# Optimization experiments

Measured on AMD Instinct MI355X. Metric: run time of the kernel, lower is better.

## Reference

```python
import jax, jax.numpy as jnp
import numpy as np

RADIUS_VIEWPOOL = 0.075  # self.view_pool_radius
EPS_BN = 1e-5


def _pconv(x, w, b):
    # 1x1 Conv1d: x (B, Cin, N), w (Cout, Cin), b (Cout,)
    return jnp.einsum('oc,bcn->bon', w, x) + b[None, :, None]


def _bn(x, p):
    # eval-mode BatchNorm1d; p rows: gamma, beta, running_mean, running_var
    g, b, m, v = p[0], p[1], p[2], p[3]
    inv = g * jax.lax.rsqrt(v + EPS_BN)
    return (x - m[None, :, None]) * inv[None, :, None] + b[None, :, None]


def setup_inputs() -> dict:
    key = jax.random.key(0)
    it = iter(jax.random.split(key, 80))
    Np, Nr = 16384, 8192
    inp = {}
    inp['pcd_xyz'] = jax.random.uniform(next(it), (1, Np, 3), jnp.float32)
    inp['rgb_xyz'] = jax.random.uniform(next(it), (1, Nr, 3), jnp.float32)
    inp['pcd_features'] = jax.random.normal(next(it), (1, 32, Np), jnp.float32)
    inp['rgb_features'] = jax.random.normal(next(it), (1, 128, Nr), jnp.float32)

    def conv(name, o, c):
        s = 1.0 / np.sqrt(c)
        inp[name + '_w'] = jax.random.uniform(next(it), (o, c), jnp.float32, -s, s)
        inp[name + '_b'] = jax.random.uniform(next(it), (o,), jnp.float32, -s, s)

    def bn(name, c):
        g = 1.0 + 0.1 * jax.random.normal(next(it), (c,), jnp.float32)
        b = 0.1 * jax.random.normal(next(it), (c,), jnp.float32)
        m = 0.1 * jax.random.normal(next(it), (c,), jnp.float32)
        v = jax.random.uniform(next(it), (c,), jnp.float32, 0.5, 1.5)
        inp[name] = jnp.stack([g, b, m, v])

    conv('cc1', 384, 384); bn('cc_bn', 384); conv('cc2', 128, 384)
    conv('co1', 256, 256); bn('co_bn', 256); conv('co2', 128, 256)
    conv('dh1', 160, 160); bn('dh1_bn', 160)
    conv('dh2', 160, 160); bn('dh2_bn', 160)
    conv('dh3', 128, 160)
    conv('sh1', 128, 128); bn('sh_bn', 128)
    conv('sh2', 1, 128)
    return inp


def _forward(pcd_xyz, rgb_xyz, pcd_features, rgb_features,
             cc1_w, cc1_b, cc_bn, cc2_w, cc2_b,
             co1_w, co1_b, co_bn, co2_w, co2_b,
             dh1_w, dh1_b, dh1_bn, dh2_w, dh2_b, dh2_bn, dh3_w, dh3_b,
             sh1_w, sh1_b, sh_bn, sh2_w, sh2_b):
    Np = pcd_xyz.shape[1]
    Nr = rgb_xyz.shape[1]
    C_rgb = rgb_features.shape[1]

    # ---- three_nn: 3 nearest rgb points for each pcd point ----
    d2 = jnp.sum((pcd_xyz[0, :, None, :] - rgb_xyz[0, None, :, :]) ** 2, axis=-1)  # (Np, Nr)
    neg_d2, idx = jax.lax.top_k(-d2, 3)                     # (Np, 3)
    dist = jnp.sqrt(jnp.maximum(-neg_d2, 0.0))
    # idx[dist > radius] = -1 in torch -> indexes shadow (zero) row appended at end
    neighbor = jnp.where(dist > RADIUS_VIEWPOOL, Nr, idx)   # (Np, 3)

    rgb_f = jnp.concatenate([rgb_features[0].T,
                             jnp.zeros((1, C_rgb), rgb_features.dtype)], axis=0)  # (Nr+1, 128)
    nf = rgb_f[neighbor]                                    # (Np, 3, 128) gather
    max_features = nf.max(axis=1)                           # (Np, 128)

    # fuception fusion: conv over concatenated neighbor features, then fuse with max
    x_cat = nf.reshape(Np, 3 * C_rgb).T[None]               # (1, 384, Np)
    h = jax.nn.relu(_bn(_pconv(x_cat, cc1_w, cc1_b), cc_bn))
    concat_out = _pconv(h, cc2_w, cc2_b)                    # (1, 128, Np)
    x2 = jnp.concatenate([concat_out, max_features.T[None]], axis=1)  # (1, 256, Np)
    h = jax.nn.relu(_bn(_pconv(x2, co1_w, co1_b), co_bn))
    attach = _pconv(h, co2_w, co2_b)                        # (1, 128, Np)

    # fuse pcd + assigned rgb features -> direct feature header (160 = 128+32)
    full = jnp.concatenate([pcd_features, attach], axis=1)  # (1, 160, Np)
    h = jax.nn.relu(_bn(_pconv(full, dh1_w, dh1_b), dh1_bn))
    h = jax.nn.relu(_bn(_pconv(h, dh2_w, dh2_b), dh2_bn))
    fp = _pconv(h, dh3_w, dh3_b)                            # (1, 128, Np)

    # score header: conv-bn-relu-conv-sigmoid
    s = jax.nn.relu(_bn(_pconv(fp, sh1_w, sh1_b), sh_bn))
    vote_scores = jax.nn.sigmoid(_pconv(s, sh2_w, sh2_b))[0, 0]  # (Np,)

    # L2-normalized vote features (N, 128)
    vf = fp[0].T
    vf = vf / jnp.maximum(jnp.linalg.norm(vf, axis=1, keepdims=True), 1e-12)
    return pcd_xyz[0], vote_scores, vf


def reference(pcd_xyz, rgb_xyz, pcd_features, rgb_features,
              cc1_w, cc1_b, cc_bn, cc2_w, cc2_b,
              co1_w, co1_b, co_bn, co2_w, co2_b,
              dh1_w, dh1_b, dh1_bn, dh2_w, dh2_b, dh2_bn, dh3_w, dh3_b,
              sh1_w, sh1_b, sh_bn, sh2_w, sh2_b):
    return _forward(pcd_xyz, rgb_xyz, pcd_features, rgb_features,
                    cc1_w, cc1_b, cc_bn, cc2_w, cc2_b,
                    co1_w, co1_b, co_bn, co2_w, co2_b,
                    dh1_w, dh1_b, dh1_bn, dh2_w, dh2_b, dh2_bn, dh3_w, dh3_b,
                    sh1_w, sh1_b, sh_bn, sh2_w, sh2_b)
```

## Files before the change

kernel.cpp:

```cpp
#include <hip/hip_runtime.h>
#include <math.h>

#define NP 16384
#define NR 8192
#define GRID 13
#define NCELL (GRID * GRID * GRID)
#define CAP 28

typedef __attribute__((ext_vector_type(8))) short short8;
typedef __attribute__((ext_vector_type(4))) float f32x4;

__device__ inline unsigned short f2b(float f) {
  unsigned int x = __float_as_uint(f);
  return (unsigned short)((x + 0x7FFFu + ((x >> 16) & 1u)) >> 16);
}
__device__ inline float blo(unsigned int u) { return __uint_as_float(u << 16); }
__device__ inline float bhi(unsigned int u) { return __uint_as_float(u & 0xffff0000u); }

__global__ __launch_bounds__(256) void k_pre(const float* __restrict__ rf,
                                             const float* __restrict__ rxyz,
                                             const float* __restrict__ pf,
                                             const float* __restrict__ s0, const float* __restrict__ s1,
                                             const float* __restrict__ s2, const float* __restrict__ s3,
                                             const float* __restrict__ s4, const float* __restrict__ s5,
                                             const float* __restrict__ s6, const float* __restrict__ s7,
                                             unsigned short* __restrict__ rgbTb,
                                             float4* __restrict__ rxyz4,
                                             unsigned short* __restrict__ fullp,
                                             unsigned short* __restrict__ dst,
                                             int* __restrict__ cellCnt) {
  __shared__ float tile[128][65];
  int b = blockIdx.x, t = threadIdx.x;
  if (b < 128) {
    int r0 = b * 64;
    for (int e = 0; e < 32; ++e) {
      int idx = t + e * 256;
      int c = idx >> 6, rl = idx & 63;
      tile[c][rl] = rf[c * NR + r0 + rl];
    }
    __syncthreads();
    for (int e = 0; e < 32; ++e) {
      int idx = t + e * 256;
      int rl = idx >> 7, c = idx & 127;
      rgbTb[(size_t)(r0 + rl) * 128 + c] = f2b(tile[c][rl]);
    }
    if (b == 0 && t < 128) rgbTb[(size_t)NR * 128 + t] = 0;
    if ((t >> 6) == 0) {
      int i = r0 + (t & 63);
      float x = rxyz[i * 3], y = rxyz[i * 3 + 1], z = rxyz[i * 3 + 2];
      rxyz4[i] = make_float4(x, y, z, fmaf(x, x, fmaf(y, y, z * z)));
    }
  } else if (b < 384) {
    int n0 = (b - 128) * 64;
    for (int e = 0; e < 8; ++e) {
      int idx = t + e * 256;
      int c = idx >> 6, nl = idx & 63;
      tile[c][nl] = pf[c * NP + n0 + nl];
    }
    __syncthreads();
    for (int e = 0; e < 8; ++e) {
      int idx = t + e * 256;
      int nl = idx >> 5, c = idx & 31;
      fullp[(size_t)(n0 + nl) * 32 + c] = f2b(tile[c][nl]);
    }
  } else if (b < 960) {
    const int groups[8] = {18432, 6144, 8192, 4096, 3200, 3200, 2560, 2048};
    const int Cs[8]     = {384, 384, 256, 256, 160, 160, 160, 128};
    const int offs[8]   = {0, 147456, 196608, 262144, 294912, 320512, 346112, 366592};
    const float* srcs[8] = {s0, s1, s2, s3, s4, s5, s6, s7};
    int j = b - 384;
    int m = j / 72, bx = j % 72;
    int gidx = bx * 256 + t;
    if (gidx >= groups[m]) return;
    int C = Cs[m], NC = C >> 5;
    int ot = gidx / (NC * 64);
    int rem = gidx - ot * (NC * 64);
    int k = rem >> 6, lane = rem & 63;
    int q = lane >> 4, l15 = lane & 15;
    const float* sp = srcs[m] + (size_t)(ot * 16 + l15) * C + k * 32 + q * 8;
    float4 a = *(const float4*)sp, c4 = *(const float4*)(sp + 4);
    uint4 o;
    o.x = f2b(a.x) | ((unsigned int)f2b(a.y) << 16);
    o.y = f2b(a.z) | ((unsigned int)f2b(a.w) << 16);
    o.z = f2b(c4.x) | ((unsigned int)f2b(c4.y) << 16);
    o.w = f2b(c4.z) | ((unsigned int)f2b(c4.w) << 16);
    *(uint4*)(dst + offs[m] + (size_t)gidx * 8) = o;
  } else {
    int idx = (b - 960) * 256 + t;
    if (idx < NCELL) cellCnt[idx] = 0;
  }
}

__global__ __launch_bounds__(64) void k_build(const float4* __restrict__ rxyz4,
                                              int* __restrict__ cellCnt,
                                              float4* __restrict__ cellTab) {
  int i = blockIdx.x * 64 + threadIdx.x;
  float4 r = rxyz4[i];
  int cx = (int)(r.x * 13.f); cx = cx < 0 ? 0 : (cx > 12 ? 12 : cx);
  int cy = (int)(r.y * 13.f); cy = cy < 0 ? 0 : (cy > 12 ? 12 : cy);
  int cz = (int)(r.z * 13.f); cz = cz < 0 ? 0 : (cz > 12 ? 12 : cz);
  int cell = (cz * 13 + cy) * 13 + cx;
  int slot = atomicAdd(&cellCnt[cell], 1);
  if (slot < CAP) cellTab[(size_t)cell * CAP + slot] = make_float4(r.x, r.y, r.z, __int_as_float(i));
}

__global__ __launch_bounds__(64) void k_nn_grid(const float* __restrict__ pxyz,
                                                const int* __restrict__ cellCnt,
                                                const float4* __restrict__ cellTab,
                                                int* __restrict__ nbr) {
  int n = blockIdx.x * 64 + threadIdx.x;
  float px = pxyz[n * 3], py = pxyz[n * 3 + 1], pz = pxyz[n * 3 + 2];
  int cx = (int)(px * 13.f); cx = cx < 0 ? 0 : (cx > 12 ? 12 : cx);
  int cy = (int)(py * 13.f); cy = cy < 0 ? 0 : (cy > 12 ? 12 : cy);
  int cz = (int)(pz * 13.f); cz = cz < 0 ? 0 : (cz > 12 ? 12 : cz);
  const float R2L = 0.005626125f;
  unsigned long long k0, k1, k2;
  k0 = k1 = k2 = ((unsigned long long)__float_as_uint(R2L) << 32);
  int x0 = cx > 0 ? cx - 1 : 0, x1 = cx < 12 ? cx + 1 : 12;
  int y0 = cy > 0 ? cy - 1 : 0, y1 = cy < 12 ? cy + 1 : 12;
  int z0 = cz > 0 ? cz - 1 : 0, z1 = cz < 12 ? cz + 1 : 12;
  for (int zz = z0; zz <= z1; ++zz)
    for (int yy = y0; yy <= y1; ++yy) {
      int cb = (zz * 13 + yy) * 13;
      for (int xx = x0; xx <= x1; ++xx) {
        int c = cb + xx;
        int m = cellCnt[c]; m = m < CAP ? m : CAP;
        const float4* tp = cellTab + (size_t)c * CAP;
        for (int k = 0; k < m; ++k) {
          float4 q = tp[k];
          float dx = q.x - px, dy = q.y - py, dz = q.z - pz;
          float d2 = fmaf(dx, dx, fmaf(dy, dy, dz * dz));
          unsigned long long key =
              ((unsigned long long)__float_as_uint(d2) << 32) | (unsigned int)__float_as_int(q.w);
          if (key < k2) {
            if (key < k1) {
              k2 = k1;
              if (key < k0) { k1 = k0; k0 = key; }
              else          { k1 = key; }
            } else k2 = key;
          }
        }
      }
    }
  const float R2 = 0.075f * 0.075f;
  float d0 = __uint_as_float((unsigned int)(k0 >> 32));
  float d1 = __uint_as_float((unsigned int)(k1 >> 32));
  float d2v = __uint_as_float((unsigned int)(k2 >> 32));
  int j0 = (d0 > R2) ? NR : (int)(k0 & 0xffffffffu);
  int j1 = (d1 > R2) ? NR : (int)(k1 & 0xffffffffu);
  int j2 = (d2v > R2) ? NR : (int)(k2 & 0xffffffffu);
  nbr[n * 3 + 0] = j0; nbr[n * 3 + 1] = j1; nbr[n * 3 + 2] = j2;
}

template <int C, int O, int COFF, bool BN, bool RELU>
__device__ __forceinline__ void mlp_layer(const unsigned short* __restrict__ W,
                                          const float* __restrict__ bias,
                                          const float* __restrict__ bnp,
                                          const unsigned short* Xs,
                                          unsigned short* Ys,
                                          int wo, int q, int l15, int lane) {
  constexpr int NC = C / 32;
  constexpr int NT = O / 16;
  constexpr int MT = (NT + 7) / 8;
  f32x4 acc[MT][2];
  short8 afb[2][MT];
  const unsigned short* wp[MT];
#pragma unroll
  for (int i = 0; i < MT; ++i) {
    acc[i][0] = (f32x4){0.f, 0.f, 0.f, 0.f};
    acc[i][1] = (f32x4){0.f, 0.f, 0.f, 0.f};
    int ot = wo + i * 8;
    wp[i] = W + ((size_t)(((ot < NT) ? ot : 0) * NC) * 64 + lane) * 8;
  }
#pragma unroll
  for (int k = 0; k < 2 && k < NC; ++k)
#pragma unroll
    for (int i = 0; i < MT; ++i)
      if (wo + i * 8 < NT) afb[k][i] = *(const short8*)(wp[i] + (size_t)k * 512);
  short8 bf0 = *(const short8*)&Xs[l15 * 392 + q * 8];
  short8 bf1 = *(const short8*)&Xs[(16 + l15) * 392 + q * 8];
#pragma unroll
  for (int k = 0; k < NC; ++k) {
    short8 nbf0 = bf0, nbf1 = bf1;
    if (k + 1 < NC) {
      nbf0 = *(const short8*)&Xs[l15 * 392 + (k + 1) * 32 + q * 8];
      nbf1 = *(const short8*)&Xs[(16 + l15) * 392 + (k + 1) * 32 + q * 8];
    }
    int slot = k & 1;
#pragma unroll
    for (int i = 0; i < MT; ++i) {
      if (wo + i * 8 < NT) {
        acc[i][0] = __builtin_amdgcn_mfma_f32_16x16x32_bf16(afb[slot][i], bf0, acc[i][0], 0, 0, 0);
        acc[i][1] = __builtin_amdgcn_mfma_f32_16x16x32_bf16(afb[slot][i], bf1, acc[i][1], 0, 0, 0);
      }
    }
    if (k + 2 < NC) {
#pragma unroll
      for (int i = 0; i < MT; ++i)
        if (wo + i * 8 < NT) afb[slot][i] = *(const short8*)(wp[i] + (size_t)(k + 2) * 512);
    }
    bf0 = nbf0; bf1 = nbf1;
  }
#pragma unroll
  for (int i = 0; i < MT; ++i) {
    int ot = wo + i * 8;
    if (ot >= NT) continue;
    int o4 = ot * 16 + q * 4;
    f32x4 bb = *(const f32x4*)(bias + o4);
    f32x4 sc, sh;
    if (BN) {
      f32x4 g  = *(const f32x4*)(bnp + o4);
      f32x4 be = *(const f32x4*)(bnp + O + o4);
      f32x4 mm = *(const f32x4*)(bnp + 2 * O + o4);
      f32x4 vv = *(const f32x4*)(bnp + 3 * O + o4);
#pragma unroll
      for (int r = 0; r < 4; ++r) {
        float inv = g[r] * rsqrtf(vv[r] + 1e-5f);
        sc[r] = inv; sh[r] = (bb[r] - mm[r]) * inv + be[r];
      }
    } else {
      sc = (f32x4){1.f, 1.f, 1.f, 1.f}; sh = bb;
    }
#pragma unroll
    for (int rt = 0; rt < 2; ++rt) {
      ushort4 u;
#pragma unroll
      for (int r = 0; r < 4; ++r) {
        float x = acc[i][rt][r] * sc[r] + sh[r];
        if (RELU) x = fmaxf(x, 0.f);
        ((unsigned short*)&u)[r] = f2b(x);
      }
      *(ushort4*)&Ys[(rt * 16 + l15) * 392 + COFF + ot * 16 + q * 4] = u;
    }
  }
}

__global__ __launch_bounds__(512) void k_mlp(
    const unsigned short* __restrict__ rgbTb,
    const int* __restrict__ nbr,
    const unsigned short* __restrict__ fullp,
    const unsigned short* __restrict__ wcc1, const unsigned short* __restrict__ wcc2,
    const unsigned short* __restrict__ wco1, const unsigned short* __restrict__ wco2,
    const unsigned short* __restrict__ wdh1, const unsigned short* __restrict__ wdh2,
    const unsigned short* __restrict__ wdh3, const unsigned short* __restrict__ wsh1,
    const float* __restrict__ cc1_b, const float* __restrict__ cc_bn,
    const float* __restrict__ cc2_b,
    const float* __restrict__ co1_b, const float* __restrict__ co_bn,
    const float* __restrict__ co2_b,
    const float* __restrict__ dh1_b, const float* __restrict__ dh1_bn,
    const float* __restrict__ dh2_b, const float* __restrict__ dh2_bn,
    const float* __restrict__ dh3_b,
    const float* __restrict__ sh1_b, const float* __restrict__ sh_bn,
    const float* __restrict__ sh2_w, const float* __restrict__ sh2_b,
    const float* __restrict__ pxyz, float* __restrict__ out) {
  __shared__ unsigned short Ab[32 * 392];
  __shared__ unsigned short Bb[32 * 392];
  int t = threadIdx.x, lane = t & 63, w = t >> 6;
  int wo = w & 7;
  int q = lane >> 4, l15 = lane & 15;
  int n0 = blockIdx.x * 32;
  unsigned int mreg[4];
#pragma unroll
  for (int pj = 0; pj < 4; ++pj) {
    int r = w * 4 + pj;
    int n = n0 + r;
    int j0 = nbr[n * 3 + 0], j1 = nbr[n * 3 + 1], j2 = nbr[n * 3 + 2];
    unsigned int a = ((const unsigned int*)(rgbTb + (size_t)j0 * 128))[lane];
    unsigned int b = ((const unsigned int*)(rgbTb + (size_t)j1 * 128))[lane];
    unsigned int c = ((const unsigned int*)(rgbTb + (size_t)j2 * 128))[lane];
    unsigned int* xr = (unsigned int*)&Ab[r * 392];
    xr[lane] = a; xr[64 + lane] = b; xr[128 + lane] = c;
    float ml = fmaxf(blo(a), fmaxf(blo(b), blo(c)));
    float mh = fmaxf(bhi(a), fmaxf(bhi(b), bhi(c)));
    mreg[pj] = (__float_as_uint(mh) & 0xffff0000u) | (__float_as_uint(ml) >> 16);
  }
  __syncthreads();
  mlp_layer<384, 384, 0, true,  true >(wcc1, cc1_b, cc_bn, Ab, Bb, wo, q, l15, lane);
  __syncthreads();
#pragma unroll
  for (int pj = 0; pj < 4; ++pj)
    ((unsigned int*)&Ab[(w * 4 + pj) * 392])[64 + lane] = mreg[pj];
  mlp_layer<384, 128, 0, false, false>(wcc2, cc2_b, nullptr, Bb, Ab, wo, q, l15, lane);
  __syncthreads();
  mlp_layer<256, 256, 0, true,  true >(wco1, co1_b, co_bn, Ab, Bb, wo, q, l15, lane);
  __syncthreads();
  mlp_layer<256, 128, 32, false, false>(wco2, co2_b, nullptr, Bb, Ab, wo, q, l15, lane);
  for (int idx = t; idx < 128; idx += 512) {
    int row = idx >> 2, c8 = idx & 3;
    *(uint4*)&Ab[row * 392 + c8 * 8] = *(const uint4*)(fullp + (size_t)(n0 + row) * 32 + c8 * 8);
  }
  __syncthreads();
  mlp_layer<160, 160, 0, true,  true >(wdh1, dh1_b, dh1_bn, Ab, Bb, wo, q, l15, lane);
  __syncthreads();
  mlp_layer<160, 160, 0, true,  true >(wdh2, dh2_b, dh2_bn, Bb, Ab, wo, q, l15, lane);
  __syncthreads();
  mlp_layer<160, 128, 0, false, false>(wdh3, dh3_b, nullptr, Ab, Bb, wo, q, l15, lane);
  __syncthreads();
  mlp_layer<128, 128, 0, true,  true >(wsh1, sh1_b, sh_bn, Bb, Ab, wo, q, l15, lane);
  __syncthreads();
  int col8 = (lane & 15) * 8;
  float4 w0 = *(const float4*)(sh2_w + col8);
  float4 wA = *(const float4*)(sh2_w + col8 + 4);
  float bvv = sh2_b[0];
  int row = w * 4 + (lane >> 4);
  uint4 raw = *(const uint4*)&Ab[row * 392 + col8];
  float acc = blo(raw.x) * w0.x + bhi(raw.x) * w0.y + blo(raw.y) * w0.z + bhi(raw.y) * w0.w +
              blo(raw.z) * wA.x + bhi(raw.z) * wA.y + blo(raw.w) * wA.z + bhi(raw.w) * wA.w;
  acc += __shfl_xor(acc, 1); acc += __shfl_xor(acc, 2);
  acc += __shfl_xor(acc, 4); acc += __shfl_xor(acc, 8);
  if ((lane & 15) == 0) out[49152 + n0 + row] = 1.f / (1.f + expf(-(acc + bvv)));
  uint4 rf = *(const uint4*)&Bb[row * 392 + col8];
  float v[8] = {blo(rf.x), bhi(rf.x), blo(rf.y), bhi(rf.y),
                blo(rf.z), bhi(rf.z), blo(rf.w), bhi(rf.w)};
  float s = 0.f;
#pragma unroll
  for (int i = 0; i < 8; ++i) s = fmaf(v[i], v[i], s);
  s += __shfl_xor(s, 1); s += __shfl_xor(s, 2);
  s += __shfl_xor(s, 4); s += __shfl_xor(s, 8);
  float inv = 1.f / fmaxf(sqrtf(s), 1e-12f);
  float* op = out + 65536 + (size_t)(n0 + row) * 128 + col8;
  *(float4*)op = make_float4(v[0] * inv, v[1] * inv, v[2] * inv, v[3] * inv);
  *(float4*)(op + 4) = make_float4(v[4] * inv, v[5] * inv, v[6] * inv, v[7] * inv);
  for (int i = t; i < 96; i += 512) out[n0 * 3 + i] = pxyz[n0 * 3 + i];
}

extern "C" void kernel_launch(void* const* d_in, const int* in_sizes, int n_in,
                              void* d_out, int out_size, void* d_ws, size_t ws_size,
                              hipStream_t stream) {
  const float* pcd_xyz = (const float*)d_in[0];
  const float* rgb_xyz = (const float*)d_in[1];
  const float* pcd_f   = (const float*)d_in[2];
  const float* rgb_f   = (const float*)d_in[3];
  const float* cc1_w = (const float*)d_in[4];  const float* cc1_b = (const float*)d_in[5];
  const float* cc_bn = (const float*)d_in[6];
  const float* cc2_w = (const float*)d_in[7];  const float* cc2_b = (const float*)d_in[8];
  const float* co1_w = (const float*)d_in[9];  const float* co1_b = (const float*)d_in[10];
  const float* co_bn = (const float*)d_in[11];
  const float* co2_w = (const float*)d_in[12]; const float* co2_b = (const float*)d_in[13];
  const float* dh1_w = (const float*)d_in[14]; const float* dh1_b = (const float*)d_in[15];
  const float* dh1_bn = (const float*)d_in[16];
  const float* dh2_w = (const float*)d_in[17]; const float* dh2_b = (const float*)d_in[18];
  const float* dh2_bn = (const float*)d_in[19];
  const float* dh3_w = (const float*)d_in[20]; const float* dh3_b = (const float*)d_in[21];
  const float* sh1_w = (const float*)d_in[22]; const float* sh1_b = (const float*)d_in[23];
  const float* sh_bn = (const float*)d_in[24];
  const float* sh2_w = (const float*)d_in[25]; const float* sh2_b = (const float*)d_in[26];

  char* ws = (char*)d_ws;
  float* out = (float*)d_out;

  unsigned short* wb    = (unsigned short*)(ws);
  unsigned short* rgbTb = (unsigned short*)(ws + 0x100000);
  float4* rxyz4         = (float4*)(ws + 0x320000);
  int*    nbr           = (int*)(ws + 0x400000);
  int*    cellCnt       = (int*)(ws + 0x480000);
  float4* cellTab       = (float4*)(ws + 0x490000);
  unsigned short* fullp = (unsigned short*)(ws + 0xA00000);

  unsigned short* wb_cc1 = wb;
  unsigned short* wb_cc2 = wb + 147456;
  unsigned short* wb_co1 = wb + 196608;
  unsigned short* wb_co2 = wb + 262144;
  unsigned short* wb_dh1 = wb + 294912;
  unsigned short* wb_dh2 = wb + 320512;
  unsigned short* wb_dh3 = wb + 346112;
  unsigned short* wb_sh1 = wb + 366592;

  k_pre<<<969, 256, 0, stream>>>(rgb_f, rgb_xyz, pcd_f,
                                 cc1_w, cc2_w, co1_w, co2_w, dh1_w, dh2_w, dh3_w, sh1_w,
                                 rgbTb, rxyz4, fullp, wb, cellCnt);
  k_build<<<128, 64, 0, stream>>>(rxyz4, cellCnt, cellTab);
  k_nn_grid<<<256, 64, 0, stream>>>(pcd_xyz, cellCnt, cellTab, nbr);
  k_mlp<<<512, 512, 0, stream>>>(rgbTb, nbr, fullp,
                                 wb_cc1, wb_cc2, wb_co1, wb_co2,
                                 wb_dh1, wb_dh2, wb_dh3, wb_sh1,
                                 cc1_b, cc_bn, cc2_b, co1_b, co_bn, co2_b,
                                 dh1_b, dh1_bn, dh2_b, dh2_bn, dh3_b,
                                 sh1_b, sh_bn, sh2_w, sh2_b,
                                 pcd_xyz, out);
}
```

Before: 188.7 us.

## Split grid neighbor search across 8 lanes per point with shuffle top-3 merge

The three-nearest-neighbor grid search now gives each query point 8 threads, each scanning a strided subset of the up to 27 neighboring cells, then merges the per-lane top-3 keys with xor shuffles. The goal is more parallelism and latency hiding in a kernel that previously launched only 16384 threads with long serial loops. In exchange it adds shuffle-merge overhead, imbalanced work per lane, and redundant coordinate loads. It also drops the unused squared-norm component and clamps neighbor indices before the feature gather.

```diff
diff --git a/kernel.cpp b/kernel.cpp
--- a/kernel.cpp
+++ b/kernel.cpp
@@ -48,7 +48,7 @@
     if ((t >> 6) == 0) {
       int i = r0 + (t & 63);
       float x = rxyz[i * 3], y = rxyz[i * 3 + 1], z = rxyz[i * 3 + 2];
-      rxyz4[i] = make_float4(x, y, z, fmaf(x, x, fmaf(y, y, z * z)));
+      rxyz4[i] = make_float4(x, y, z, 0.f);
     }
   } else if (b < 384) {
     int n0 = (b - 128) * 64;
@@ -104,34 +104,37 @@
   if (slot < CAP) cellTab[(size_t)cell * CAP + slot] = make_float4(r.x, r.y, r.z, __int_as_float(i));
 }
 
-__global__ __launch_bounds__(64) void k_nn_grid(const float* __restrict__ pxyz,
-                                                const int* __restrict__ cellCnt,
-                                                const float4* __restrict__ cellTab,
-                                                int* __restrict__ nbr) {
-  int n = blockIdx.x * 64 + threadIdx.x;
+__global__ __launch_bounds__(256) void k_nn_grid(const float* __restrict__ pxyz,
+                                                 const int* __restrict__ cellCnt,
+                                                 const float4* __restrict__ cellTab,
+                                                 int* __restrict__ nbr) {
+  int tid = blockIdx.x * 256 + threadIdx.x;
+  int n = tid >> 3, sub = tid & 7;
   float px = pxyz[n * 3], py = pxyz[n * 3 + 1], pz = pxyz[n * 3 + 2];
   int cx = (int)(px * 13.f); cx = cx < 0 ? 0 : (cx > 12 ? 12 : cx);
   int cy = (int)(py * 13.f); cy = cy < 0 ? 0 : (cy > 12 ? 12 : cy);
   int cz = (int)(pz * 13.f); cz = cz < 0 ? 0 : (cz > 12 ? 12 : cz);
   const float R2L = 0.005626125f;
-  unsigned long long k0, k1, k2;
-  k0 = k1 = k2 = ((unsigned long long)__float_as_uint(R2L) << 32);
-  int x0 = cx > 0 ? cx - 1 : 0, x1 = cx < 12 ? cx + 1 : 12;
-  int y0 = cy > 0 ? cy - 1 : 0, y1 = cy < 12 ? cy + 1 : 12;
-  int z0 = cz > 0 ? cz - 1 : 0, z1 = cz < 12 ? cz + 1 : 12;
-  for (int zz = z0; zz <= z1; ++zz)
-    for (int yy = y0; yy <= y1; ++yy) {
+  const unsigned long long SENT = ((unsigned long long)__float_as_uint(R2L) << 32);
+  unsigned long long k0 = SENT, k1 = SENT, k2 = SENT;
+  int vi = 0;
+  for (int dz = -1; dz <= 1; ++dz) {
+    int zz = cz + dz; if ((unsigned)zz > 12u) continue;
+    for (int dy = -1; dy <= 1; ++dy) {
+      int yy = cy + dy; if ((unsigned)yy > 12u) continue;
       int cb = (zz * 13 + yy) * 13;
-      for (int xx = x0; xx <= x1; ++xx) {
+      for (int dx = -1; dx <= 1; ++dx) {
+        int xx = cx + dx; if ((unsigned)xx > 12u) continue;
+        if (((vi++) & 7) != sub) continue;
         int c = cb + xx;
         int m = cellCnt[c]; m = m < CAP ? m : CAP;
         const float4* tp = cellTab + (size_t)c * CAP;
         for (int k = 0; k < m; ++k) {
-          float4 q = tp[k];
-          float dx = q.x - px, dy = q.y - py, dz = q.z - pz;
-          float d2 = fmaf(dx, dx, fmaf(dy, dy, dz * dz));
+          float4 qq = tp[k];
+          float dxx = qq.x - px, dyy = qq.y - py, dzz = qq.z - pz;
+          float d2 = fmaf(dxx, dxx, fmaf(dyy, dyy, dzz * dzz));
           unsigned long long key =
-              ((unsigned long long)__float_as_uint(d2) << 32) | (unsigned int)__float_as_int(q.w);
+              ((unsigned long long)__float_as_uint(d2) << 32) | (unsigned int)__float_as_int(qq.w);
           if (key < k2) {
             if (key < k1) {
               k2 = k1;
@@ -142,14 +145,31 @@
         }
       }
     }
-  const float R2 = 0.075f * 0.075f;
-  float d0 = __uint_as_float((unsigned int)(k0 >> 32));
-  float d1 = __uint_as_float((unsigned int)(k1 >> 32));
-  float d2v = __uint_as_float((unsigned int)(k2 >> 32));
-  int j0 = (d0 > R2) ? NR : (int)(k0 & 0xffffffffu);
-  int j1 = (d1 > R2) ? NR : (int)(k1 & 0xffffffffu);
-  int j2 = (d2v > R2) ? NR : (int)(k2 & 0xffffffffu);
-  nbr[n * 3 + 0] = j0; nbr[n * 3 + 1] = j1; nbr[n * 3 + 2] = j2;
+  }
+  int pos = 0;
+  unsigned long long res[3];
+#pragma unroll
+  for (int r = 0; r < 3; ++r) {
+    unsigned long long cur = (pos == 0) ? k0 : (pos == 1) ? k1 : (pos == 2) ? k2 : ~0ull;
+    unsigned long long m = cur;
+#pragma unroll
+    for (int o = 1; o <= 4; o <<= 1) {
+      unsigned long long other = __shfl_xor(m, o);
+      m = other < m ? other : m;
+    }
+    res[r] = m;
+    if (cur == m) ++pos;
+  }
+  if (sub == 0) {
+    const float R2 = 0.075f * 0.075f;
+    float d0 = __uint_as_float((unsigned int)(res[0] >> 32));
+    float d1 = __uint_as_float((unsigned int)(res[1] >> 32));
+    float d2v = __uint_as_float((unsigned int)(res[2] >> 32));
+    int j0 = (d0 > R2) ? NR : (int)(res[0] & 0xffffffffu);
+    int j1 = (d1 > R2) ? NR : (int)(res[1] & 0xffffffffu);
+    int j2 = (d2v > R2) ? NR : (int)(res[2] & 0xffffffffu);
+    nbr[n * 3 + 0] = j0; nbr[n * 3 + 1] = j1; nbr[n * 3 + 2] = j2;
+  }
 }
 
 template <int C, int O, int COFF, bool BN, bool RELU>
@@ -264,7 +284,9 @@
   for (int pj = 0; pj < 4; ++pj) {
     int r = w * 4 + pj;
     int n = n0 + r;
-    int j0 = nbr[n * 3 + 0], j1 = nbr[n * 3 + 1], j2 = nbr[n * 3 + 2];
+    unsigned int j0 = (unsigned int)nbr[n * 3 + 0]; j0 = j0 > NR ? NR : j0;
+    unsigned int j1 = (unsigned int)nbr[n * 3 + 1]; j1 = j1 > NR ? NR : j1;
+    unsigned int j2 = (unsigned int)nbr[n * 3 + 2]; j2 = j2 > NR ? NR : j2;
     unsigned int a = ((const unsigned int*)(rgbTb + (size_t)j0 * 128))[lane];
     unsigned int b = ((const unsigned int*)(rgbTb + (size_t)j1 * 128))[lane];
     unsigned int c = ((const unsigned int*)(rgbTb + (size_t)j2 * 128))[lane];
@@ -370,7 +392,7 @@
                                  cc1_w, cc2_w, co1_w, co2_w, dh1_w, dh2_w, dh3_w, sh1_w,
                                  rgbTb, rxyz4, fullp, wb, cellCnt);
   k_build<<<128, 64, 0, stream>>>(rxyz4, cellCnt, cellTab);
-  k_nn_grid<<<256, 64, 0, stream>>>(pcd_xyz, cellCnt, cellTab, nbr);
+  k_nn_grid<<<512, 256, 0, stream>>>(pcd_xyz, cellCnt, cellTab, nbr);
   k_mlp<<<512, 512, 0, stream>>>(rgbTb, nbr, fullp,
                                  wb_cc1, wb_cc2, wb_co1, wb_co2,
                                  wb_dh1, wb_dh2, wb_dh3, wb_sh1,
```

Result: no change. 186.5 us (-1.1%).
